# Kernel tuning notes

Hardware: AMD Instinct MI355X
Metric: run time of the kernel (lower is better)

## Reference

```python
import jax, jax.numpy as jnp
import numpy as np

N, E, F_IN, HID, HEADS, OUT, G = 50000, 800000, 128, 64, 4, 10, 64
NEG_SLOPE = 0.2


def _glorot(key, shape):
    fan = shape[0] + shape[-1]
    lim = np.sqrt(6.0 / fan)
    return jax.random.uniform(key, shape, jnp.float32, -lim, lim)


def setup_inputs() -> dict:
    key = jax.random.key(0)
    ks = jax.random.split(key, 20)
    x = jax.random.normal(ks[0], (N, F_IN), jnp.float32)
    edge_index = jax.random.randint(ks[1], (2, E), 0, N, jnp.int64)
    batch = jnp.sort(jax.random.randint(ks[2], (N,), 0, G, jnp.int64))
    inp = {"x": x, "edge_index": edge_index, "batch": batch}
    # layer 1: in=F_IN, heads=HEADS, out=HID
    inp["W1"] = _glorot(ks[3], (F_IN, HEADS * HID))
    inp["b1"] = jnp.zeros((HEADS * HID,), jnp.float32)
    inp["as1"] = _glorot(ks[4], (HEADS, HID))
    inp["ad1"] = _glorot(ks[5], (HEADS, HID))
    # layer 2: in=HEADS*HID, heads=HEADS, out=HID
    inp["W2"] = _glorot(ks[6], (HEADS * HID, HEADS * HID))
    inp["b2"] = jnp.zeros((HEADS * HID,), jnp.float32)
    inp["as2"] = _glorot(ks[7], (HEADS, HID))
    inp["ad2"] = _glorot(ks[8], (HEADS, HID))
    # layer 3: in=HEADS*HID, heads=1, out=HID
    inp["W3"] = _glorot(ks[9], (HEADS * HID, HID))
    inp["b3"] = jnp.zeros((HID,), jnp.float32)
    inp["as3"] = _glorot(ks[10], (1, HID))
    inp["ad3"] = _glorot(ks[11], (1, HID))
    # MLP head [HID, HID, OUT]
    inp["Wm1"] = _glorot(ks[12], (HID, HID))
    inp["bm1"] = jnp.zeros((HID,), jnp.float32)
    inp["Wm2"] = _glorot(ks[13], (HID, OUT))
    inp["bm2"] = jnp.zeros((OUT,), jnp.float32)
    return inp


def _gat_layer(x, src, dst, W, b, att_src, att_dst):
    # x: [N, Fin]; att_*: [H, C]
    H, C = att_src.shape
    h = (x @ W).reshape(N, H, C)
    a_src = jnp.einsum("nhc,hc->nh", h, att_src)
    a_dst = jnp.einsum("nhc,hc->nh", h, att_dst)
    alpha = jax.nn.leaky_relu(a_src[src] + a_dst[dst], NEG_SLOPE)  # [E', H]
    amax = jax.ops.segment_max(alpha, dst, num_segments=N)
    alpha = jnp.exp(alpha - amax[dst])
    denom = jax.ops.segment_sum(alpha, dst, num_segments=N)
    alpha = alpha / (denom[dst] + 1e-16)
    msg = h[src] * alpha[:, :, None]  # [E', H, C]
    out = jax.ops.segment_sum(msg, dst, num_segments=N)  # [N, H, C]
    return out.reshape(N, H * C) + b


def reference(x, edge_index, batch, W1, b1, as1, ad1, W2, b2, as2, ad2, W3, b3, as3, ad3, Wm1, bm1, Wm2, bm2):
    # PyG GATConv adds self-loops by default
    loops = jnp.arange(N, dtype=edge_index.dtype)
    src = jnp.concatenate([edge_index[0], loops])
    dst = jnp.concatenate([edge_index[1], loops])
    h = jax.nn.relu(_gat_layer(x, src, dst, W1, b1, as1, ad1))
    h = jax.nn.relu(_gat_layer(h, src, dst, W2, b2, as2, ad2))
    h = jax.nn.relu(_gat_layer(h, src, dst, W3, b3, as3, ad3))
    pooled = jax.ops.segment_sum(h, batch, num_segments=G)  # [G, HID]
    hidden = jax.nn.relu(pooled @ Wm1 + bm1)
    return hidden @ Wm2 + bm2
```

## Files before the change

### kernel.cpp

```cpp
#include <hip/hip_runtime.h>
#include <hip/hip_bf16.h>

#define F_IN   128
#define HID    64
#define HEADS  4
#define OUTD   10
#define NGRP   64

typedef unsigned short u16;
typedef __attribute__((ext_vector_type(8))) short short8;
typedef __attribute__((ext_vector_type(4))) float f32x4;

__device__ __forceinline__ float atomAddF(float* p, float v) {
    return __hip_atomic_fetch_add(p, v, __ATOMIC_RELAXED, __HIP_MEMORY_SCOPE_AGENT);
}
__device__ __forceinline__ float lrelu(float f) { return f > 0.f ? f : 0.2f * f; }
__device__ __forceinline__ float b2f(u16 u) { return __uint_as_float(((unsigned)u) << 16); }
__device__ __forceinline__ u16 f2b(float f) {
    unsigned u = __float_as_uint(f);
    return (u16)((u + 0x7fffu + ((u >> 16) & 1u)) >> 16);
}
__device__ __forceinline__ unsigned fmono(float f) {
    unsigned u = __float_as_uint(f);
    return (u & 0x80000000u) ? ~u : (u | 0x80000000u);
}
__device__ __forceinline__ float funmono(unsigned u) {
    return __uint_as_float((u & 0x80000000u) ? (u & 0x7FFFFFFFu) : ~u);
}

__global__ __launch_bounds__(256) void wtrans_all_kernel(const float* __restrict__ W1,
                                                         const float* __restrict__ W2,
                                                         const float* __restrict__ W3,
                                                         u16* __restrict__ Wt1,
                                                         u16* __restrict__ Wt2,
                                                         u16* __restrict__ Wt3) {
    int i = blockIdx.x * 256 + threadIdx.x;
    if (i < 32768) {
        int n = i >> 7, k = i & 127;
        Wt1[i] = f2b(W1[(size_t)k * 256 + n]);
    } else if (i < 98304) {
        int j = i - 32768;
        int n = j >> 8, k = j & 255;
        Wt2[j] = f2b(W2[(size_t)k * 256 + n]);
    } else if (i < 114688) {
        int j = i - 98304;
        int n = j >> 8, k = j & 255;
        Wt3[j] = f2b(W3[(size_t)k * 64 + n]);
    }
}

template<int K, int NC, bool AF32>
__global__ __launch_bounds__(256) void gemm_att_kernel(const void* __restrict__ Aptr,
                                                       const u16* __restrict__ Bt,
                                                       const float* __restrict__ as_,
                                                       const float* __restrict__ ad_,
                                                       u16* __restrict__ Hb,
                                                       float* __restrict__ a_src,
                                                       float* __restrict__ a_dst,
                                                       int nrows) {
    constexpr int LDA = 40;
    constexpr int HH = NC / 64;
    __shared__ u16 As[64][LDA];
    __shared__ u16 Bs[NC][LDA];
    int tid = threadIdx.x;
    int m0 = blockIdx.x * 64;
    int w = tid >> 6, l = tid & 63, lr = l & 15, lk = l >> 4;

    if constexpr (NC == 256) {
        f32x4 acc[4][4] = {};
        for (int k0 = 0; k0 < K; k0 += 32) {
            {
                int row = tid >> 2, ks = (tid & 3) * 8;
                int grow = m0 + row;
                short8 av = {};
                if (grow < nrows) {
                    if constexpr (AF32) {
                        const float* src = (const float*)Aptr + (size_t)grow * K + k0 + ks;
                        float4 v0 = *(const float4*)src;
                        float4 v1 = *(const float4*)(src + 4);
                        av[0] = (short)f2b(v0.x); av[1] = (short)f2b(v0.y);
                        av[2] = (short)f2b(v0.z); av[3] = (short)f2b(v0.w);
                        av[4] = (short)f2b(v1.x); av[5] = (short)f2b(v1.y);
                        av[6] = (short)f2b(v1.z); av[7] = (short)f2b(v1.w);
                    } else {
                        av = *(const short8*)&((const u16*)Aptr)[(size_t)grow * K + k0 + ks];
                    }
                }
                *(short8*)&As[row][ks] = av;
            }
            #pragma unroll
            for (int i = 0; i < 4; i++) {
                int col = (tid >> 2) + 64 * i;
                int ks = (tid & 3) * 8;
                *(short8*)&Bs[col][ks] = *(const short8*)&Bt[(size_t)col * K + k0 + ks];
            }
            __syncthreads();
            short8 a[4], b[4];
            #pragma unroll
            for (int mi = 0; mi < 4; mi++) a[mi] = *(const short8*)&As[16 * mi + lr][lk * 8];
            #pragma unroll
            for (int ni = 0; ni < 4; ni++) b[ni] = *(const short8*)&Bs[64 * w + 16 * ni + lr][lk * 8];
            #pragma unroll
            for (int mi = 0; mi < 4; mi++)
                #pragma unroll
                for (int ni = 0; ni < 4; ni++)
                    acc[mi][ni] = __builtin_amdgcn_mfma_f32_16x16x32_bf16(a[mi], b[ni], acc[mi][ni], 0, 0, 0);
            __syncthreads();
        }
        #pragma unroll
        for (int mi = 0; mi < 4; mi++) {
            #pragma unroll
            for (int j = 0; j < 4; j++) {
                int grow = m0 + 16 * mi + lk * 4 + j;
                if (grow < nrows) {
                    #pragma unroll
                    for (int ni = 0; ni < 4; ni++)
                        Hb[(size_t)grow * NC + 64 * w + 16 * ni + lr] = f2b(acc[mi][ni][j]);
                }
            }
        }
        float asv[4], adv[4];
        #pragma unroll
        for (int ni = 0; ni < 4; ni++) {
            asv[ni] = as_[w * 64 + 16 * ni + lr];
            adv[ni] = ad_[w * 64 + 16 * ni + lr];
        }
        #pragma unroll
        for (int mi = 0; mi < 4; mi++) {
            #pragma unroll
            for (int j = 0; j < 4; j++) {
                float ps = 0.f, pd = 0.f;
                #pragma unroll
                for (int ni = 0; ni < 4; ni++) {
                    float v = acc[mi][ni][j];
                    ps += v * asv[ni];
                    pd += v * adv[ni];
                }
                #pragma unroll
                for (int o = 1; o < 16; o <<= 1) {
                    ps += __shfl_xor(ps, o, 64);
                    pd += __shfl_xor(pd, o, 64);
                }
                int grow = m0 + 16 * mi + lk * 4 + j;
                if (lr == 0 && grow < nrows) {
                    a_src[grow * HH + w] = ps;
                    a_dst[grow * HH + w] = pd;
                }
            }
        }
    } else {
        f32x4 acc[4] = {};
        for (int k0 = 0; k0 < K; k0 += 32) {
            {
                int row = tid >> 2, ks = (tid & 3) * 8;
                int grow = m0 + row;
                short8 av = {};
                if (grow < nrows) av = *(const short8*)&((const u16*)Aptr)[(size_t)grow * K + k0 + ks];
                *(short8*)&As[row][ks] = av;
            }
            {
                int col = tid >> 2;
                int ks = (tid & 3) * 8;
                *(short8*)&Bs[col][ks] = *(const short8*)&Bt[(size_t)col * K + k0 + ks];
            }
            __syncthreads();
            short8 af = *(const short8*)&As[16 * w + lr][lk * 8];
            #pragma unroll
            for (int c = 0; c < 4; c++) {
                short8 bf = *(const short8*)&Bs[c * 16 + lr][lk * 8];
                acc[c] = __builtin_amdgcn_mfma_f32_16x16x32_bf16(af, bf, acc[c], 0, 0, 0);
            }
            __syncthreads();
        }
        #pragma unroll
        for (int c = 0; c < 4; c++) {
            #pragma unroll
            for (int j = 0; j < 4; j++) {
                int grow = m0 + 16 * w + lk * 4 + j;
                if (grow < nrows) Hb[(size_t)grow * NC + c * 16 + lr] = f2b(acc[c][j]);
            }
        }
        float asv[4], adv[4];
        #pragma unroll
        for (int c = 0; c < 4; c++) {
            asv[c] = as_[c * 16 + lr];
            adv[c] = ad_[c * 16 + lr];
        }
        #pragma unroll
        for (int j = 0; j < 4; j++) {
            float ps = 0.f, pd = 0.f;
            #pragma unroll
            for (int c = 0; c < 4; c++) {
                float v = acc[c][j];
                ps += v * asv[c];
                pd += v * adv[c];
            }
            #pragma unroll
            for (int o = 1; o < 16; o <<= 1) {
                ps += __shfl_xor(ps, o, 64);
                pd += __shfl_xor(pd, o, 64);
            }
            int grow = m0 + 16 * w + lk * 4 + j;
            if (lr == 0 && grow < nrows) {
                a_src[grow] = ps;
                a_dst[grow] = pd;
            }
        }
    }
}

template<int HH>
__global__ __launch_bounds__(256) void gmax_kernel(const float* __restrict__ a_src,
                                                   unsigned* __restrict__ gmaxu, int n_nodes) {
    float mx[HH];
    #pragma unroll
    for (int h = 0; h < HH; h++) mx[h] = -3.4e38f;
    for (int i = blockIdx.x * 256 + threadIdx.x; i < n_nodes; i += gridDim.x * 256) {
        #pragma unroll
        for (int h = 0; h < HH; h++) mx[h] = fmaxf(mx[h], a_src[i * HH + h]);
    }
    #pragma unroll
    for (int h = 0; h < HH; h++) {
        #pragma unroll
        for (int off = 32; off; off >>= 1) mx[h] = fmaxf(mx[h], __shfl_xor(mx[h], off, 64));
    }
    if ((threadIdx.x & 63) == 0) {
        #pragma unroll
        for (int h = 0; h < HH; h++) atomicMax(&gmaxu[h], fmono(mx[h]));
    }
}

__global__ void count_kernel(const int* __restrict__ ei, int* __restrict__ deg,
                             int E_, int n_nodes) {
    int e = blockIdx.x * 256 + threadIdx.x;
    int tot = E_ + n_nodes;
    if (e >= tot) return;
    int d = (e < E_) ? ei[E_ + e] : e - E_;
    atomicAdd(&deg[d], 1);
}

__global__ __launch_bounds__(256) void scan_reduce_kernel(const int* __restrict__ deg,
                                                          int* __restrict__ bsum, int n) {
    int i = blockIdx.x * 256 + threadIdx.x;
    int v = (i < n) ? deg[i] : 0;
    #pragma unroll
    for (int o = 32; o; o >>= 1) v += __shfl_xor(v, o, 64);
    __shared__ int ws[4];
    if ((threadIdx.x & 63) == 0) ws[threadIdx.x >> 6] = v;
    __syncthreads();
    if (threadIdx.x == 0) bsum[blockIdx.x] = ws[0] + ws[1] + ws[2] + ws[3];
}

__global__ __launch_bounds__(256) void scan_blocksums_kernel(int* __restrict__ bsum, int nb) {
    __shared__ int s[256];
    int t = threadIdx.x;
    int v = (t < nb) ? bsum[t] : 0;
    s[t] = v;
    __syncthreads();
    #pragma unroll
    for (int d = 1; d < 256; d <<= 1) {
        int x = (t >= d) ? s[t - d] : 0;
        __syncthreads();
        s[t] += x;
        __syncthreads();
    }
    if (t < nb) bsum[t] = s[t] - v;
}

__global__ __launch_bounds__(256) void scan_final_kernel(const int* __restrict__ deg,
                                                         const int* __restrict__ bsum,
                                                         int* __restrict__ off, int n) {
    __shared__ int s[256];
    int t = threadIdx.x;
    int i = blockIdx.x * 256 + t;
    int v = (i < n) ? deg[i] : 0;
    s[t] = v;
    __syncthreads();
    #pragma unroll
    for (int d = 1; d < 256; d <<= 1) {
        int x = (t >= d) ? s[t - d] : 0;
        __syncthreads();
        s[t] += x;
        __syncthreads();
    }
    int ex = s[t] - v + bsum[blockIdx.x];
    if (i < n) off[i] = ex;
    if (i == n - 1) off[n] = ex + v;
}

__global__ void fill_kernel(const int* __restrict__ ei, const int* __restrict__ off,
                            int* __restrict__ cursor, int* __restrict__ csr_src,
                            int E_, int n_nodes) {
    int e = blockIdx.x * 256 + threadIdx.x;
    int tot = E_ + n_nodes;
    if (e >= tot) return;
    int s, d;
    if (e < E_) { s = ei[e]; d = ei[E_ + e]; } else { s = d = e - E_; }
    int pos = atomicAdd(&cursor[d], 1);
    csr_src[off[d] + pos] = s;
}

template<int HH, int CPL, bool OUTF32>
__global__ __launch_bounds__(256) void gat_aggr_kernel(const int* __restrict__ off,
                                                       const int* __restrict__ csr_src,
                                                       const u16* __restrict__ Hb,
                                                       const float* __restrict__ a_src,
                                                       const float* __restrict__ a_dst,
                                                       const unsigned* __restrict__ gmaxu,
                                                       const float* __restrict__ bias,
                                                       u16* __restrict__ outb16,
                                                       float* __restrict__ outf32,
                                                       int n_nodes) {
    constexpr int HC = 64 * CPL;
    constexpr int GRP = 64 / HH;
    int d = blockIdx.x * 4 + (threadIdx.x >> 6);
    if (d >= n_nodes) return;
    int lane = threadIdx.x & 63;
    int hh = lane / GRP;
    int g = lane & (GRP - 1);
    int gb = lane & (64 - GRP);
    int o0 = off[d];
    int deg = off[d + 1] - o0;
    float adm = a_dst[d * HH + hh];
    float m = lrelu(funmono(gmaxu[hh]) + adm);

    float den = 0.f;
    float acc[CPL] = {};
    int j = 0;
    for (; j + 8 <= deg; j += 8) {
        int s[8];
        #pragma unroll
        for (int t = 0; t < 8; t++) s[t] = csr_src[o0 + j + t];
        int ssel = s[g & 7];
        float e = __expf(lrelu(a_src[ssel * HH + hh] + adm) - m);
        float ee[8];
        #pragma unroll
        for (int t = 0; t < 8; t++) ee[t] = __shfl(e, gb + t, 64);
        #pragma unroll
        for (int t = 0; t < 8; t++) den += ee[t];
        if constexpr (CPL == 4) {
            uint2 hv[8];
            #pragma unroll
            for (int t = 0; t < 8; t++) hv[t] = *(const uint2*)&Hb[(size_t)s[t] * HC + lane * 4];
            #pragma unroll
            for (int t = 0; t < 8; t++) {
                acc[0] += ee[t] * __uint_as_float(hv[t].x << 16);
                acc[1] += ee[t] * __uint_as_float(hv[t].x & 0xffff0000u);
                acc[2] += ee[t] * __uint_as_float(hv[t].y << 16);
                acc[3] += ee[t] * __uint_as_float(hv[t].y & 0xffff0000u);
            }
        } else {
            u16 hv[8];
            #pragma unroll
            for (int t = 0; t < 8; t++) hv[t] = Hb[(size_t)s[t] * HC + lane];
            #pragma unroll
            for (int t = 0; t < 8; t++) acc[0] += ee[t] * b2f(hv[t]);
        }
    }
    for (; j < deg; j++) {
        int s = csr_src[o0 + j];
        float al = __expf(lrelu(a_src[s * HH + hh] + adm) - m);
        den += al;
        if constexpr (CPL == 4) {
            uint2 hv = *(const uint2*)&Hb[(size_t)s * HC + lane * 4];
            acc[0] += al * __uint_as_float(hv.x << 16);
            acc[1] += al * __uint_as_float(hv.x & 0xffff0000u);
            acc[2] += al * __uint_as_float(hv.y << 16);
            acc[3] += al * __uint_as_float(hv.y & 0xffff0000u);
        } else {
            acc[0] += al * b2f(Hb[(size_t)s * HC + lane]);
        }
    }
    float inv = 1.f / (den + 1e-16f);
    if constexpr (CPL == 4) {
        float4 bv = *(const float4*)&bias[lane * 4];
        float v0 = fmaxf(acc[0] * inv + bv.x, 0.f);
        float v1 = fmaxf(acc[1] * inv + bv.y, 0.f);
        float v2 = fmaxf(acc[2] * inv + bv.z, 0.f);
        float v3 = fmaxf(acc[3] * inv + bv.w, 0.f);
        uint2 o;
        o.x = (unsigned)f2b(v0) | ((unsigned)f2b(v1) << 16);
        o.y = (unsigned)f2b(v2) | ((unsigned)f2b(v3) << 16);
        *(uint2*)&outb16[(size_t)d * HC + lane * 4] = o;
    } else {
        float v = fmaxf(acc[0] * inv + bias[lane], 0.f);
        if constexpr (OUTF32) outf32[(size_t)d * HC + lane] = v;
        else                  outb16[(size_t)d * HC + lane] = f2b(v);
    }
}

__global__ __launch_bounds__(256) void pool_kernel(const float* __restrict__ H3,
                                                   const int* __restrict__ batch,
                                                   float* __restrict__ pooled, int n_nodes) {
    int wave = (blockIdx.x * 256 + threadIdx.x) >> 6;
    int lane = threadIdx.x & 63;
    int nwaves = gridDim.x * 4;
    int chunk = (n_nodes + nwaves - 1) / nwaves;
    int start = wave * chunk;
    int end = min(n_nodes, start + chunk);
    if (start >= end) return;
    int cur = batch[start];
    float acc = 0.f;
    for (int n = start; n < end; n++) {
        int g = batch[n];
        if (g != cur) { atomAddF(&pooled[cur * 64 + lane], acc); acc = 0.f; cur = g; }
        acc += H3[(size_t)n * 64 + lane];
    }
    atomAddF(&pooled[cur * 64 + lane], acc);
}

__global__ __launch_bounds__(64) void mlp_kernel(const float* __restrict__ pooled,
                                                 const float* __restrict__ Wm1,
                                                 const float* __restrict__ bm1,
                                                 const float* __restrict__ Wm2,
                                                 const float* __restrict__ bm2,
                                                 float* __restrict__ out) {
    __shared__ float sp[64], sh[64];
    int g = blockIdx.x, t = threadIdx.x;
    sp[t] = pooled[g * 64 + t];
    __syncthreads();
    float a = bm1[t];
    for (int k = 0; k < 64; k++) a += sp[k] * Wm1[k * 64 + t];
    sh[t] = a > 0.f ? a : 0.f;
    __syncthreads();
    if (t < 10) {
        float o = bm2[t];
        for (int j = 0; j < 64; j++) o += sh[j] * Wm2[j * 10 + t];
        out[g * 10 + t] = o;
    }
}

extern "C" void kernel_launch(void* const* d_in, const int* in_sizes, int n_in,
                              void* d_out, int out_size, void* d_ws, size_t ws_size,
                              hipStream_t stream) {
    const float* x   = (const float*)d_in[0];
    const int*   ei  = (const int*)d_in[1];
    const int*   bat = (const int*)d_in[2];
    const float* W1  = (const float*)d_in[3];
    const float* b1  = (const float*)d_in[4];
    const float* as1 = (const float*)d_in[5];
    const float* ad1 = (const float*)d_in[6];
    const float* W2  = (const float*)d_in[7];
    const float* b2  = (const float*)d_in[8];
    const float* as2 = (const float*)d_in[9];
    const float* ad2 = (const float*)d_in[10];
    const float* W3  = (const float*)d_in[11];
    const float* b3  = (const float*)d_in[12];
    const float* as3 = (const float*)d_in[13];
    const float* ad3 = (const float*)d_in[14];
    const float* Wm1 = (const float*)d_in[15];
    const float* bm1 = (const float*)d_in[16];
    const float* Wm2 = (const float*)d_in[17];
    const float* bm2 = (const float*)d_in[18];
    float* out = (float*)d_out;

    const int Nn = in_sizes[0] / F_IN;
    const int Ee = in_sizes[1] / 2;
    const int Et = Ee + Nn;

    char* wsp = (char*)d_ws;
    size_t off_b = 0;
    auto alloc = [&](size_t bytes) { void* p = wsp + off_b; off_b += (bytes + 255) & ~(size_t)255; return p; };
    u16*   HbA     = (u16*)alloc((size_t)Nn * 256 * 2);
    u16*   HbB     = (u16*)alloc((size_t)Nn * 256 * 2);
    float* Hf      = (float*)alloc((size_t)Nn * HID * 4);
    u16*   Wt1     = (u16*)alloc((size_t)256 * 128 * 2);
    u16*   Wt2     = (u16*)alloc((size_t)256 * 256 * 2);
    u16*   Wt3     = (u16*)alloc((size_t)64 * 256 * 2);
    float* a_src   = (float*)alloc((size_t)Nn * HEADS * 4);
    float* a_dst   = (float*)alloc((size_t)Nn * HEADS * 4);
    unsigned* gmaxu = (unsigned*)alloc(16 * 4);
    int*   deg     = (int*)alloc((size_t)Nn * 2 * 4);
    int*   cursor  = deg + Nn;
    int*   bsum    = (int*)alloc((size_t)256 * 4);
    int*   csr_off = (int*)alloc((size_t)(Nn + 1) * 4);
    int*   csr_src = (int*)alloc((size_t)Et * 4);
    float* pooled  = (float*)alloc((size_t)NGRP * HID * 4);
    (void)ws_size;

    wtrans_all_kernel<<<(114688 + 255) / 256, 256, 0, stream>>>(W1, W2, W3, Wt1, Wt2, Wt3);

    hipMemsetAsync(deg, 0, (size_t)Nn * 2 * 4, stream);
    hipMemsetAsync(gmaxu, 0, 16 * 4, stream);
    int eb = (Et + 255) / 256;
    int nb = (Nn + 255) / 256;
    count_kernel<<<eb, 256, 0, stream>>>(ei, deg, Ee, Nn);
    scan_reduce_kernel<<<nb, 256, 0, stream>>>(deg, bsum, Nn);
    scan_blocksums_kernel<<<1, 256, 0, stream>>>(bsum, nb);
    scan_final_kernel<<<nb, 256, 0, stream>>>(deg, bsum, csr_off, Nn);
    fill_kernel<<<eb, 256, 0, stream>>>(ei, csr_off, cursor, csr_src, Ee, Nn);

    const int gemm_blocks = (Nn + 63) / 64;
    const int nodeBlocks = (Nn + 3) / 4;

    gemm_att_kernel<128, 256, true><<<gemm_blocks, 256, 0, stream>>>(x, Wt1, as1, ad1,
                                                                     HbA, a_src, a_dst, Nn);
    gmax_kernel<4><<<64, 256, 0, stream>>>(a_src, gmaxu + 0, Nn);
    gat_aggr_kernel<4, 4, false><<<nodeBlocks, 256, 0, stream>>>(csr_off, csr_src, HbA,
                                                                 a_src, a_dst, gmaxu + 0, b1,
                                                                 HbB, nullptr, Nn);
    gemm_att_kernel<256, 256, false><<<gemm_blocks, 256, 0, stream>>>(HbB, Wt2, as2, ad2,
                                                                      HbA, a_src, a_dst, Nn);
    gmax_kernel<4><<<64, 256, 0, stream>>>(a_src, gmaxu + 4, Nn);
    gat_aggr_kernel<4, 4, false><<<nodeBlocks, 256, 0, stream>>>(csr_off, csr_src, HbA,
                                                                 a_src, a_dst, gmaxu + 4, b2,
                                                                 HbB, nullptr, Nn);
    gemm_att_kernel<256, 64, false><<<gemm_blocks, 256, 0, stream>>>(HbB, Wt3, as3, ad3,
                                                                     HbA, a_src, a_dst, Nn);
    gmax_kernel<1><<<64, 256, 0, stream>>>(a_src, gmaxu + 8, Nn);
    gat_aggr_kernel<1, 1, true><<<nodeBlocks, 256, 0, stream>>>(csr_off, csr_src, HbA,
                                                                a_src, a_dst, gmaxu + 8, b3,
                                                                nullptr, Hf, Nn);

    hipMemsetAsync(pooled, 0, (size_t)NGRP * HID * 4, stream);
    pool_kernel<<<128, 256, 0, stream>>>(Hf, bat, pooled, Nn);
    mlp_kernel<<<NGRP, 64, 0, stream>>>(pooled, Wm1, bm1, Wm2, bm2, out);
}
```

Before: 406.0 us.

## Fuse global max into GEMM and pooling into final aggregation, merge memsets

Computes the per-head attention source max inside the GEMM epilogue with per-wave atomicMax, removing the separate gmax kernels. The final GAT aggregation atomically adds its output directly into per-graph pooled sums, eliminating the fp32 intermediate and the pool kernel. Zeroed buffers are merged into one memset, and the aggregation edge loop unroll is reduced from 8 to 4. This trades launch overhead and an intermediate buffer for heavy contended float atomics on pooled and possibly less memory-level parallelism in gathers.

After: 472.5 us. +16.4%, slower.

```diff
diff --git a/kernel.cpp b/kernel.cpp
--- a/kernel.cpp
+++ b/kernel.cpp
@@ -57,6 +57,7 @@
                                                        u16* __restrict__ Hb,
                                                        float* __restrict__ a_src,
                                                        float* __restrict__ a_dst,
+                                                       unsigned* __restrict__ gmaxu,
                                                        int nrows) {
     constexpr int LDA = 40;
     constexpr int HH = NC / 64;
@@ -125,6 +126,7 @@
             asv[ni] = as_[w * 64 + 16 * ni + lr];
             adv[ni] = ad_[w * 64 + 16 * ni + lr];
         }
+        float mxs = -3.4e38f;
         #pragma unroll
         for (int mi = 0; mi < 4; mi++) {
             #pragma unroll
@@ -141,6 +143,7 @@
                     ps += __shfl_xor(ps, o, 64);
                     pd += __shfl_xor(pd, o, 64);
                 }
+                mxs = fmaxf(mxs, ps);
                 int grow = m0 + 16 * mi + lk * 4 + j;
                 if (lr == 0 && grow < nrows) {
                     a_src[grow * HH + w] = ps;
@@ -148,6 +151,9 @@
                 }
             }
         }
+        mxs = fmaxf(mxs, __shfl_xor(mxs, 16, 64));
+        mxs = fmaxf(mxs, __shfl_xor(mxs, 32, 64));
+        if (l == 0) atomicMax(&gmaxu[w], fmono(mxs));
     } else {
         f32x4 acc[4] = {};
         for (int k0 = 0; k0 < K; k0 += 32) {
@@ -186,6 +192,7 @@
             asv[c] = as_[c * 16 + lr];
             adv[c] = ad_[c * 16 + lr];
         }
+        float mxs = -3.4e38f;
         #pragma unroll
         for (int j = 0; j < 4; j++) {
             float ps = 0.f, pd = 0.f;
@@ -200,33 +207,16 @@
                 ps += __shfl_xor(ps, o, 64);
                 pd += __shfl_xor(pd, o, 64);
             }
+            mxs = fmaxf(mxs, ps);
             int grow = m0 + 16 * w + lk * 4 + j;
             if (lr == 0 && grow < nrows) {
                 a_src[grow] = ps;
                 a_dst[grow] = pd;
             }
         }
-    }
-}
-
-template<int HH>
-__global__ __launch_bounds__(256) void gmax_kernel(const float* __restrict__ a_src,
-                                                   unsigned* __restrict__ gmaxu, int n_nodes) {
-    float mx[HH];
-    #pragma unroll
-    for (int h = 0; h < HH; h++) mx[h] = -3.4e38f;
-    for (int i = blockIdx.x * 256 + threadIdx.x; i < n_nodes; i += gridDim.x * 256) {
-        #pragma unroll
-        for (int h = 0; h < HH; h++) mx[h] = fmaxf(mx[h], a_src[i * HH + h]);
-    }
-    #pragma unroll
-    for (int h = 0; h < HH; h++) {
-        #pragma unroll
-        for (int off = 32; off; off >>= 1) mx[h] = fmaxf(mx[h], __shfl_xor(mx[h], off, 64));
-    }
-    if ((threadIdx.x & 63) == 0) {
-        #pragma unroll
-        for (int h = 0; h < HH; h++) atomicMax(&gmaxu[h], fmono(mx[h]));
+        mxs = fmaxf(mxs, __shfl_xor(mxs, 16, 64));
+        mxs = fmaxf(mxs, __shfl_xor(mxs, 32, 64));
+        if (l == 0) atomicMax(&gmaxu[0], fmono(mxs));
     }
 }
 
@@ -300,7 +290,7 @@
     csr_src[off[d] + pos] = s;
 }
 
-template<int HH, int CPL, bool OUTF32>
+template<int HH, int CPL, bool POOL>
 __global__ __launch_bounds__(256) void gat_aggr_kernel(const int* __restrict__ off,
                                                        const int* __restrict__ csr_src,
                                                        const u16* __restrict__ Hb,
@@ -309,7 +299,8 @@
                                                        const unsigned* __restrict__ gmaxu,
                                                        const float* __restrict__ bias,
                                                        u16* __restrict__ outb16,
-                                                       float* __restrict__ outf32,
+                                                       const int* __restrict__ batch,
+                                                       float* __restrict__ pooled,
                                                        int n_nodes) {
     constexpr int HC = 64 * CPL;
     constexpr int GRP = 64 / HH;
@@ -327,34 +318,38 @@
     float den = 0.f;
     float acc[CPL] = {};
     int j = 0;
-    for (; j + 8 <= deg; j += 8) {
-        int s[8];
-        #pragma unroll
-        for (int t = 0; t < 8; t++) s[t] = csr_src[o0 + j + t];
-        int ssel = s[g & 7];
+    for (; j + 4 <= deg; j += 4) {
+        int s0 = csr_src[o0 + j + 0];
+        int s1 = csr_src[o0 + j + 1];
+        int s2 = csr_src[o0 + j + 2];
+        int s3 = csr_src[o0 + j + 3];
+        int ssel = s3;
+        if (g == 0) ssel = s0; else if (g == 1) ssel = s1; else if (g == 2) ssel = s2;
         float e = __expf(lrelu(a_src[ssel * HH + hh] + adm) - m);
-        float ee[8];
-        #pragma unroll
-        for (int t = 0; t < 8; t++) ee[t] = __shfl(e, gb + t, 64);
-        #pragma unroll
-        for (int t = 0; t < 8; t++) den += ee[t];
+        float e0 = __shfl(e, gb + 0, 64);
+        float e1 = __shfl(e, gb + 1, 64);
+        float e2 = __shfl(e, gb + 2, 64);
+        float e3 = __shfl(e, gb + 3, 64);
+        den += (e0 + e1) + (e2 + e3);
         if constexpr (CPL == 4) {
-            uint2 hv[8];
-            #pragma unroll
-            for (int t = 0; t < 8; t++) hv[t] = *(const uint2*)&Hb[(size_t)s[t] * HC + lane * 4];
-            #pragma unroll
-            for (int t = 0; t < 8; t++) {
-                acc[0] += ee[t] * __uint_as_float(hv[t].x << 16);
-                acc[1] += ee[t] * __uint_as_float(hv[t].x & 0xffff0000u);
-                acc[2] += ee[t] * __uint_as_float(hv[t].y << 16);
-                acc[3] += ee[t] * __uint_as_float(hv[t].y & 0xffff0000u);
-            }
+            uint2 h0 = *(const uint2*)&Hb[(size_t)s0 * HC + lane * 4];
+            uint2 h1 = *(const uint2*)&Hb[(size_t)s1 * HC + lane * 4];
+            uint2 h2 = *(const uint2*)&Hb[(size_t)s2 * HC + lane * 4];
+            uint2 h3 = *(const uint2*)&Hb[(size_t)s3 * HC + lane * 4];
+            acc[0] += e0 * __uint_as_float(h0.x << 16) + e1 * __uint_as_float(h1.x << 16)
+                    + e2 * __uint_as_float(h2.x << 16) + e3 * __uint_as_float(h3.x << 16);
+            acc[1] += e0 * __uint_as_float(h0.x & 0xffff0000u) + e1 * __uint_as_float(h1.x & 0xffff0000u)
+                    + e2 * __uint_as_float(h2.x & 0xffff0000u) + e3 * __uint_as_float(h3.x & 0xffff0000u);
+            acc[2] += e0 * __uint_as_float(h0.y << 16) + e1 * __uint_as_float(h1.y << 16)
+                    + e2 * __uint_as_float(h2.y << 16) + e3 * __uint_as_float(h3.y << 16);
+            acc[3] += e0 * __uint_as_float(h0.y & 0xffff0000u) + e1 * __uint_as_float(h1.y & 0xffff0000u)
+                    + e2 * __uint_as_float(h2.y & 0xffff0000u) + e3 * __uint_as_float(h3.y & 0xffff0000u);
         } else {
-            u16 hv[8];
-            #pragma unroll
-            for (int t = 0; t < 8; t++) hv[t] = Hb[(size_t)s[t] * HC + lane];
-            #pragma unroll
-            for (int t = 0; t < 8; t++) acc[0] += ee[t] * b2f(hv[t]);
+            u16 h0 = Hb[(size_t)s0 * HC + lane];
+            u16 h1 = Hb[(size_t)s1 * HC + lane];
+            u16 h2 = Hb[(size_t)s2 * HC + lane];
+            u16 h3 = Hb[(size_t)s3 * HC + lane];
+            acc[0] += e0 * b2f(h0) + e1 * b2f(h1) + e2 * b2f(h2) + e3 * b2f(h3);
         }
     }
     for (; j < deg; j++) {
@@ -384,29 +379,12 @@
         *(uint2*)&outb16[(size_t)d * HC + lane * 4] = o;
     } else {
         float v = fmaxf(acc[0] * inv + bias[lane], 0.f);
-        if constexpr (OUTF32) outf32[(size_t)d * HC + lane] = v;
-        else                  outb16[(size_t)d * HC + lane] = f2b(v);
-    }
-}
-
-__global__ __launch_bounds__(256) void pool_kernel(const float* __restrict__ H3,
-                                                   const int* __restrict__ batch,
-                                                   float* __restrict__ pooled, int n_nodes) {
-    int wave = (blockIdx.x * 256 + threadIdx.x) >> 6;
-    int lane = threadIdx.x & 63;
-    int nwaves = gridDim.x * 4;
-    int chunk = (n_nodes + nwaves - 1) / nwaves;
-    int start = wave * chunk;
-    int end = min(n_nodes, start + chunk);
-    if (start >= end) return;
-    int cur = batch[start];
-    float acc = 0.f;
-    for (int n = start; n < end; n++) {
-        int g = batch[n];
-        if (g != cur) { atomAddF(&pooled[cur * 64 + lane], acc); acc = 0.f; cur = g; }
-        acc += H3[(size_t)n * 64 + lane];
-    }
-    atomAddF(&pooled[cur * 64 + lane], acc);
+        if constexpr (POOL) {
+            atomAddF(&pooled[(size_t)batch[d] * 64 + lane], v);
+        } else {
+            outb16[(size_t)d * HC + lane] = f2b(v);
+        }
+    }
 }
 
 __global__ __launch_bounds__(64) void mlp_kernel(const float* __restrict__ pooled,
@@ -463,25 +441,26 @@
     auto alloc = [&](size_t bytes) { void* p = wsp + off_b; off_b += (bytes + 255) & ~(size_t)255; return p; };
     u16*   HbA     = (u16*)alloc((size_t)Nn * 256 * 2);
     u16*   HbB     = (u16*)alloc((size_t)Nn * 256 * 2);
-    float* Hf      = (float*)alloc((size_t)Nn * HID * 4);
     u16*   Wt1     = (u16*)alloc((size_t)256 * 128 * 2);
     u16*   Wt2     = (u16*)alloc((size_t)256 * 256 * 2);
     u16*   Wt3     = (u16*)alloc((size_t)64 * 256 * 2);
     float* a_src   = (float*)alloc((size_t)Nn * HEADS * 4);
     float* a_dst   = (float*)alloc((size_t)Nn * HEADS * 4);
-    unsigned* gmaxu = (unsigned*)alloc(16 * 4);
-    int*   deg     = (int*)alloc((size_t)Nn * 2 * 4);
+    size_t zcount = 16 + (size_t)Nn * 2 + NGRP * HID;
+    unsigned* zbase = (unsigned*)alloc(zcount * 4);
+    unsigned* gmaxu = zbase;
+    int*   deg     = (int*)(zbase + 16);
     int*   cursor  = deg + Nn;
+    float* pooled  = (float*)(cursor + Nn);
     int*   bsum    = (int*)alloc((size_t)256 * 4);
     int*   csr_off = (int*)alloc((size_t)(Nn + 1) * 4);
     int*   csr_src = (int*)alloc((size_t)Et * 4);
-    float* pooled  = (float*)alloc((size_t)NGRP * HID * 4);
     (void)ws_size;
 
     wtrans_all_kernel<<<(114688 + 255) / 256, 256, 0, stream>>>(W1, W2, W3, Wt1, Wt2, Wt3);
 
-    hipMemsetAsync(deg, 0, (size_t)Nn * 2 * 4, stream);
-    hipMemsetAsync(gmaxu, 0, 16 * 4, stream);
+    hipMemsetAsync(zbase, 0, zcount * 4, stream);
+
     int eb = (Et + 255) / 256;
     int nb = (Nn + 255) / 256;
     count_kernel<<<eb, 256, 0, stream>>>(ei, deg, Ee, Nn);
@@ -494,25 +473,23 @@
     const int nodeBlocks = (Nn + 3) / 4;
 
     gemm_att_kernel<128, 256, true><<<gemm_blocks, 256, 0, stream>>>(x, Wt1, as1, ad1,
-                                                                     HbA, a_src, a_dst, Nn);
-    gmax_kernel<4><<<64, 256, 0, stream>>>(a_src, gmaxu + 0, Nn);
+                                                                     HbA, a_src, a_dst,
+                                                                     gmaxu + 0, Nn);
     gat_aggr_kernel<4, 4, false><<<nodeBlocks, 256, 0, stream>>>(csr_off, csr_src, HbA,
                                                                  a_src, a_dst, gmaxu + 0, b1,
-                                                                 HbB, nullptr, Nn);
+                                                                 HbB, nullptr, nullptr, Nn);
     gemm_att_kernel<256, 256, false><<<gemm_blocks, 256, 0, stream>>>(HbB, Wt2, as2, ad2,
-                                                                      HbA, a_src, a_dst, Nn);
-    gmax_kernel<4><<<64, 256, 0, stream>>>(a_src, gmaxu + 4, Nn);
+                                                                      HbA, a_src, a_dst,
+                                                                      gmaxu + 4, Nn);
     gat_aggr_kernel<4, 4, false><<<nodeBlocks, 256, 0, stream>>>(csr_off, csr_src, HbA,
                                                                  a_src, a_dst, gmaxu + 4, b2,
-                                                                 HbB, nullptr, Nn);
+                                                                 HbB, nullptr, nullptr, Nn);
     gemm_att_kernel<256, 64, false><<<gemm_blocks, 256, 0, stream>>>(HbB, Wt3, as3, ad3,
-                                                                     HbA, a_src, a_dst, Nn);
-    gmax_kernel<1><<<64, 256, 0, stream>>>(a_src, gmaxu + 8, Nn);
+                                                                     HbA, a_src, a_dst,
+                                                                     gmaxu + 8, Nn);
     gat_aggr_kernel<1, 1, true><<<nodeBlocks, 256, 0, stream>>>(csr_off, csr_src, HbA,
                                                                 a_src, a_dst, gmaxu + 8, b3,
-                                                                nullptr, Hf, Nn);
-
-    hipMemsetAsync(pooled, 0, (size_t)NGRP * HID * 4, stream);
-    pool_kernel<<<128, 256, 0, stream>>>(Hf, bat, pooled, Nn);
+                                                                nullptr, bat, pooled, Nn);
+
     mlp_kernel<<<NGRP, 64, 0, stream>>>(pooled, Wm1, bm1, Wm2, bm2, out);
 }
```
